# Kernel tuning notes

Measured on AMD Instinct MI355X. Metric: run time of the kernel, lower is better.

The kernel has to match this reference:

```python
import jax, jax.numpy as jnp
import numpy as np

BETA = 2.0  # init kwarg beta


def _roi_map(roi_params, H, W):
    # roi_params: (N, K, 4) = (mu_x, mu_y, sigma_x, sigma_y) in [0, 1]
    dtype = roi_params.dtype
    gx = (jnp.arange(W, dtype=dtype) + 0.5) / W  # x-coords of grid columns
    gy = (jnp.arange(H, dtype=dtype) + 0.5) / H  # y-coords of grid rows
    mu_x, mu_y = roi_params[:, :, 0], roi_params[:, :, 1]
    sg_x, sg_y = roi_params[:, :, 2], roi_params[:, :, 3]
    # separable generalized-Gaussian log pdf along each axis
    log_x = -(jnp.abs(gx[None, None, :] - mu_x[:, :, None]) / sg_x[:, :, None]) ** BETA  # (N,K,W)
    log_y = -(jnp.abs(gy[None, None, :] - mu_y[:, :, None]) / sg_y[:, :, None]) ** BETA  # (N,K,H)
    scores = jnp.exp(log_y[:, :, :, None] + log_x[:, :, None, :])  # (N,K,H,W)
    mx = jnp.max(scores, axis=(2, 3), keepdims=True)
    return scores / (mx + 1e-12)  # max-normalized attention maps


def setup_inputs() -> dict:
    key = jax.random.key(0)
    k1, k2 = jax.random.split(key)
    x = jax.random.normal(k1, (16, 128, 128, 256), dtype=jnp.float32)
    roi_params = jax.random.uniform(k2, (16, 64, 4), dtype=jnp.float32)
    return {"x": x, "roi_params": roi_params}


def reference(x, roi_params):
    N, H, W, d = x.shape
    roi_map = _roi_map(roi_params, H, W)           # (N,K,H,W)
    flat_map = roi_map.reshape(N, -1, H * W)        # (N,K,HW)
    flat_feats = x.reshape(N, H * W, d)             # (N,HW,d)
    roi_features = jnp.einsum('nrf,nfd->nrd', flat_map, flat_feats) / (H * W)
    return roi_features, roi_params, roi_map
```

## Files before the change

kernel.cpp:

```cpp
#include <hip/hip_runtime.h>
#include <hip/hip_bf16.h>
#include <math.h>

#define NB 16
#define RB 64
#define HB 128
#define WB 128
#define DB 256
#define HW (HB * WB)

typedef __attribute__((ext_vector_type(8))) short bf16x8;
typedef __attribute__((ext_vector_type(4))) float f32x4;

static __device__ __forceinline__ short f2bf(float f) {
  __hip_bfloat16 h = __float2bfloat16(f);
  return *reinterpret_cast<short*>(&h);
}

#define GLOAD_LDS16(gp, lp)                                          \
  __builtin_amdgcn_global_load_lds(                                  \
      (const __attribute__((address_space(1))) unsigned int*)(gp),   \
      (__attribute__((address_space(3))) unsigned int*)(lp), 16, 0, 0)

static __device__ __forceinline__ float axis_maxlog(float mu, float sg) {
  int i = (int)roundf(mu * 128.0f - 0.5f);
  i = i < 0 ? 0 : (i > 127 ? 127 : i);
  const float g = (i + 0.5f) * (1.0f / 128.0f);
  const float tm = fabsf(g - mu) / sg;
  return -(tm * tm);
}

template <bool INTERLEAVE>
__global__ __launch_bounds__(512, 1) void fused_kernel(
    const float* __restrict__ x, const float* __restrict__ roi,
    float* __restrict__ partials, float* __restrict__ out_map,
    float* __restrict__ out_params) {
  __shared__ float buf[4][32 * DB];

  const int bid = blockIdx.x;
  const int t   = threadIdx.x;

  bool is_map = false;
  int fid = bid, mb = 0;
  if constexpr (INTERLEAVE) {
    is_map = (bid % 3) == 2;
    fid    = (bid / 3) * 2 + (bid % 3);
    mb     = bid / 3;
  }

  if (is_map) {
    float* sEx = &buf[0][0];
    float* sEy = sEx + 512;
    for (int v = t; v < 1024; v += 512) {
      const int rr = v >> 8, axis = (v >> 7) & 1, pos = v & 127;
      const int nr = mb * 4 + rr;
      const float4 rp = reinterpret_cast<const float4*>(roi)[nr];
      const float mlx = axis_maxlog(rp.x, rp.z);
      const float mly = axis_maxlog(rp.y, rp.w);
      const float em  = expf(mlx + mly);
      const float s   = em / (em + 1e-12f);
      const float g   = (pos + 0.5f) * (1.0f / 128.0f);
      if (axis == 0) {
        const float tx = fabsf(g - rp.x) / rp.z;
        sEx[rr * 128 + pos] = expf(-(tx * tx) - mlx);
      } else {
        const float ty = fabsf(g - rp.y) / rp.w;
        sEy[rr * 128 + pos] = expf(-(ty * ty) - mly) * s;
      }
    }
    if (mb == 0) {
      for (int i = t; i < NB * RB * 4; i += 512) out_params[i] = roi[i];
    }
    __syncthreads();
    f32x4* dst = reinterpret_cast<f32x4*>(out_map + (size_t)mb * 4 * HW);
#pragma unroll
    for (int p = 0; p < 32; ++p) {
      const int idx = p * 512 + t;
      const int rr = idx >> 12, h = (idx >> 5) & 127, w4 = idx & 31;
      const f32x4 e = *reinterpret_cast<const f32x4*>(&sEx[rr * 128 + w4 * 4]);
      dst[idx] = e * (f32x4)sEy[rr * 128 + h];
    }
    return;
  }

  const int n   = fid >> 5;
  const int kc  = fid & 31;
  const int l   = t & 63;
  const int wv  = t >> 6;
  const int mh  = wv >> 2;
  const int dw  = wv & 3;
  const int l15 = l & 15;
  const int lk  = (l >> 4) * 8;
  const int h0  = kc * 4;
  const int dbase = dw * 64 + l15 * 4;

  const char* gx =
      (const char*)(x + ((size_t)n * HW + (size_t)kc * 512) * DB);
  char* lbase = (char*)&buf[0][0];

  f32x4 exr[2][4][2];
  float eyv[4][2];
#pragma unroll
  for (int rf = 0; rf < 2; ++rf) {
    const int nr = n * RB + mh * 32 + rf * 16 + l15;
    const float4 rp = reinterpret_cast<const float4*>(roi)[nr];
    const float mlx = axis_maxlog(rp.x, rp.z);
    const float mly = axis_maxlog(rp.y, rp.w);
    const float em  = expf(mlx + mly);
    const float s   = em / (em + 1e-12f);
#pragma unroll
    for (int ks = 0; ks < 4; ++ks) {
#pragma unroll
      for (int hf = 0; hf < 2; ++hf) {
        f32x4 v;
#pragma unroll
        for (int j = 0; j < 4; ++j) {
          const int col = ks * 32 + lk + hf * 4 + j;
          const float g = (col + 0.5f) * (1.0f / 128.0f);
          const float tx = fabsf(g - rp.x) / rp.z;
          v[j] = expf(-(tx * tx) - mlx);
        }
        exr[rf][ks][hf] = v;
      }
    }
#pragma unroll
    for (int hh = 0; hh < 4; ++hh) {
      const float g = (h0 + hh + 0.5f) * (1.0f / 128.0f);
      const float ty = fabsf(g - rp.y) / rp.w;
      eyv[hh][rf] = expf(-(ty * ty) - mly) * s;
    }
  }
  asm volatile("s_waitcnt vmcnt(0)" ::: "memory");

  f32x4 acc[2][4];
#pragma unroll
  for (int rf = 0; rf < 2; ++rf)
#pragma unroll
    for (int f = 0; f < 4; ++f) acc[rf][f] = (f32x4)0.0f;

#define STAGE(bi, slot) do {                                                 \
    const char* gsrc_ = gx + (size_t)(bi) * 32768;                           \
    char* ldst_ = lbase + (slot) * 32768;                                    \
    _Pragma("unroll")                                                        \
    for (int ii = 0; ii < 4; ++ii)                                           \
      GLOAD_LDS16(gsrc_ + ii * 8192 + wv * 1024 + l * 16,                    \
                  ldst_ + ii * 8192 + wv * 1024);                            \
  } while (0)

  STAGE(0, 0); STAGE(1, 1); STAGE(2, 2);

#define KSTEP(bi, VM, DO_STAGE) do {                                         \
    asm volatile("s_waitcnt vmcnt(" #VM ")" ::: "memory");                   \
    __builtin_amdgcn_s_barrier();                                            \
    __builtin_amdgcn_sched_barrier(0);                                       \
    if (DO_STAGE) STAGE((bi) + 3, ((bi) + 3) & 3);                           \
    const float* bp_ = &buf[(bi) & 3][0];                                    \
    f32x4 xv_[8];                                                            \
    _Pragma("unroll")                                                        \
    for (int j = 0; j < 8; ++j)                                              \
      xv_[j] = *reinterpret_cast<const f32x4*>(                              \
          bp_ + (lk + j) * DB + dbase);                                      \
    bf16x8 bfr_[4];                                                          \
    _Pragma("unroll")                                                        \
    for (int f = 0; f < 4; ++f) {                                            \
      bf16x8 b_;                                                             \
      _Pragma("unroll")                                                      \
      for (int j = 0; j < 8; ++j) b_[j] = f2bf(xv_[j][f]);                   \
      bfr_[f] = b_;                                                          \
    }                                                                        \
    bf16x8 afr_[2];                                                          \
    _Pragma("unroll")                                                        \
    for (int rf = 0; rf < 2; ++rf) {                                         \
      const float ey_ = eyv[(bi) >> 2][rf];                                  \
      const f32x4 e0_ = exr[rf][(bi) & 3][0];                                \
      const f32x4 e1_ = exr[rf][(bi) & 3][1];                                \
      bf16x8 a_;                                                             \
      a_[0] = f2bf(ey_ * e0_.x); a_[1] = f2bf(ey_ * e0_.y);                  \
      a_[2] = f2bf(ey_ * e0_.z); a_[3] = f2bf(ey_ * e0_.w);                  \
      a_[4] = f2bf(ey_ * e1_.x); a_[5] = f2bf(ey_ * e1_.y);                  \
      a_[6] = f2bf(ey_ * e1_.z); a_[7] = f2bf(ey_ * e1_.w);                  \
      afr_[rf] = a_;                                                         \
    }                                                                        \
    _Pragma("unroll")                                                        \
    for (int rf = 0; rf < 2; ++rf)                                           \
      _Pragma("unroll")                                                      \
      for (int f = 0; f < 4; ++f)                                            \
        acc[rf][f] = __builtin_amdgcn_mfma_f32_16x16x32_bf16(                \
            afr_[rf], bfr_[f], acc[rf][f], 0, 0, 0);                         \
  } while (0)

  KSTEP(0, 8, 1);  KSTEP(1, 8, 1);  KSTEP(2, 8, 1);  KSTEP(3, 8, 1);
  KSTEP(4, 8, 1);  KSTEP(5, 8, 1);  KSTEP(6, 8, 1);  KSTEP(7, 8, 1);
  KSTEP(8, 8, 1);  KSTEP(9, 8, 1);  KSTEP(10, 8, 1); KSTEP(11, 8, 1);
  KSTEP(12, 8, 1); KSTEP(13, 8, 0); KSTEP(14, 4, 0); KSTEP(15, 0, 0);

#undef KSTEP
#undef STAGE

  float* P = partials + (size_t)fid * (RB * DB);
#pragma unroll
  for (int rf = 0; rf < 2; ++rf) {
#pragma unroll
    for (int reg = 0; reg < 4; ++reg) {
      const int r = mh * 32 + rf * 16 + (l >> 4) * 4 + reg;
      f32x4 v;
      v.x = acc[rf][0][reg]; v.y = acc[rf][1][reg];
      v.z = acc[rf][2][reg]; v.w = acc[rf][3][reg];
      *reinterpret_cast<f32x4*>(P + (size_t)r * DB + dbase) = v;
    }
  }
}

__global__ __launch_bounds__(512) void map_only_kernel(
    const float* __restrict__ roi, float* __restrict__ out_map,
    float* __restrict__ out_params) {
  __shared__ float sT[1024];
  const int mb = blockIdx.x;
  const int t  = threadIdx.x;
  float* sEx = sT;
  float* sEy = sT + 512;
  for (int v = t; v < 1024; v += 512) {
    const int rr = v >> 8, axis = (v >> 7) & 1, pos = v & 127;
    const int nr = mb * 4 + rr;
    const float4 rp = reinterpret_cast<const float4*>(roi)[nr];
    const float mlx = axis_maxlog(rp.x, rp.z);
    const float mly = axis_maxlog(rp.y, rp.w);
    const float em  = expf(mlx + mly);
    const float s   = em / (em + 1e-12f);
    const float g   = (pos + 0.5f) * (1.0f / 128.0f);
    if (axis == 0) {
      const float tx = fabsf(g - rp.x) / rp.z;
      sEx[rr * 128 + pos] = expf(-(tx * tx) - mlx);
    } else {
      const float ty = fabsf(g - rp.y) / rp.w;
      sEy[rr * 128 + pos] = expf(-(ty * ty) - mly) * s;
    }
  }
  if (mb == 0) {
    for (int i = t; i < NB * RB * 4; i += 512) out_params[i] = roi[i];
  }
  __syncthreads();
  f32x4* dst = reinterpret_cast<f32x4*>(out_map + (size_t)mb * 4 * HW);
#pragma unroll
  for (int p = 0; p < 32; ++p) {
    const int idx = p * 512 + t;
    const int rr = idx >> 12, h = (idx >> 5) & 127, w4 = idx & 31;
    const f32x4 e = *reinterpret_cast<const f32x4*>(&sEx[rr * 128 + w4 * 4]);
    dst[idx] = e * (f32x4)sEy[rr * 128 + h];
  }
}

__global__ __launch_bounds__(256) void reduce_kernel(
    const float* __restrict__ partials, float* __restrict__ outF) {
  const int idx = blockIdx.x * 256 + threadIdx.x;
  const int n   = idx >> 12;
  const int i4  = idx & 4095;
  const f32x4* p =
      reinterpret_cast<const f32x4*>(partials) + (size_t)n * 32 * 4096 + i4;
  f32x4 s0 = (f32x4)0.0f, s1 = (f32x4)0.0f, s2 = (f32x4)0.0f, s3 = (f32x4)0.0f;
#pragma unroll
  for (int kc = 0; kc < 32; kc += 4) {
    s0 += p[(size_t)(kc + 0) * 4096];
    s1 += p[(size_t)(kc + 1) * 4096];
    s2 += p[(size_t)(kc + 2) * 4096];
    s3 += p[(size_t)(kc + 3) * 4096];
  }
  f32x4 s = (s0 + s1) + (s2 + s3);
  s *= (1.0f / (float)HW);
  reinterpret_cast<f32x4*>(outF)[idx] = s;
}

extern "C" void kernel_launch(void* const* d_in, const int* in_sizes, int n_in,
                              void* d_out, int out_size, void* d_ws, size_t ws_size,
                              hipStream_t stream) {
  const float* x   = (const float*)d_in[0];
  const float* roi = (const float*)d_in[1];
  float* out        = (float*)d_out;
  float* ws         = (float*)d_ws;
  float* out_feat   = out;
  float* out_params = out + NB * RB * DB;
  float* out_map    = out_params + NB * RB * 4;

  const size_t par_floats = 512u * RB * DB;
  const bool ws_ok = ws_size >= (par_floats + 16) * sizeof(float);

  if (ws_ok) {
    float* P = ws;
    fused_kernel<true><<<768, 512, 0, stream>>>(x, roi, P, out_map, out_params);
    reduce_kernel<<<256, 256, 0, stream>>>(P, out_feat);
  } else {
    float* P = out_map;
    fused_kernel<false><<<512, 512, 0, stream>>>(x, roi, P, out_map, out_params);
    reduce_kernel<<<256, 256, 0, stream>>>(P, out_feat);
    map_only_kernel<<<256, 512, 0, stream>>>(roi, out_map, out_params);
  }
}
```

Baseline: 99.12 us.

## Halve split-K blocks, emit map inside GEMM blocks, store bf16 partials

Drops the split-K factor from 32 to 16 chunks per batch, so 256 blocks each process 1024 spatial positions. Each GEMM block now writes its own 8 rows of the attention map after finishing its matmul, replacing the separate interleaved map-only blocks. Partials are stored as bf16, halving workspace traffic, and the params copy moves into the reduce kernel. The trade-offs are rounding error in the bf16 partial sums, and map writes serialized after the GEMM with fewer blocks than CUs available to overlap them.

```diff
diff --git a/kernel.cpp b/kernel.cpp
--- a/kernel.cpp
+++ b/kernel.cpp
@@ -10,11 +10,15 @@
 #define HW (HB * WB)
 
 typedef __attribute__((ext_vector_type(8))) short bf16x8;
+typedef __attribute__((ext_vector_type(4))) short short4v;
 typedef __attribute__((ext_vector_type(4))) float f32x4;
 
 static __device__ __forceinline__ short f2bf(float f) {
   __hip_bfloat16 h = __float2bfloat16(f);
   return *reinterpret_cast<short*>(&h);
+}
+static __device__ __forceinline__ float bf2f(short s) {
+  return __uint_as_float(((unsigned)(unsigned short)s) << 16);
 }
 
 #define GLOAD_LDS16(gp, lp)                                          \
@@ -30,76 +34,31 @@
   return -(tm * tm);
 }
 
-template <bool INTERLEAVE>
+template <bool WMAP>
 __global__ __launch_bounds__(512, 1) void fused_kernel(
     const float* __restrict__ x, const float* __restrict__ roi,
-    float* __restrict__ partials, float* __restrict__ out_map,
-    float* __restrict__ out_params) {
+    short* __restrict__ partials, float* __restrict__ out_map) {
   __shared__ float buf[4][32 * DB];
 
   const int bid = blockIdx.x;
+  const int n   = bid >> 4;
+  const int kc  = bid & 15;
   const int t   = threadIdx.x;
-
-  bool is_map = false;
-  int fid = bid, mb = 0;
-  if constexpr (INTERLEAVE) {
-    is_map = (bid % 3) == 2;
-    fid    = (bid / 3) * 2 + (bid % 3);
-    mb     = bid / 3;
-  }
-
-  if (is_map) {
-    float* sEx = &buf[0][0];
-    float* sEy = sEx + 512;
-    for (int v = t; v < 1024; v += 512) {
-      const int rr = v >> 8, axis = (v >> 7) & 1, pos = v & 127;
-      const int nr = mb * 4 + rr;
-      const float4 rp = reinterpret_cast<const float4*>(roi)[nr];
-      const float mlx = axis_maxlog(rp.x, rp.z);
-      const float mly = axis_maxlog(rp.y, rp.w);
-      const float em  = expf(mlx + mly);
-      const float s   = em / (em + 1e-12f);
-      const float g   = (pos + 0.5f) * (1.0f / 128.0f);
-      if (axis == 0) {
-        const float tx = fabsf(g - rp.x) / rp.z;
-        sEx[rr * 128 + pos] = expf(-(tx * tx) - mlx);
-      } else {
-        const float ty = fabsf(g - rp.y) / rp.w;
-        sEy[rr * 128 + pos] = expf(-(ty * ty) - mly) * s;
-      }
-    }
-    if (mb == 0) {
-      for (int i = t; i < NB * RB * 4; i += 512) out_params[i] = roi[i];
-    }
-    __syncthreads();
-    f32x4* dst = reinterpret_cast<f32x4*>(out_map + (size_t)mb * 4 * HW);
-#pragma unroll
-    for (int p = 0; p < 32; ++p) {
-      const int idx = p * 512 + t;
-      const int rr = idx >> 12, h = (idx >> 5) & 127, w4 = idx & 31;
-      const f32x4 e = *reinterpret_cast<const f32x4*>(&sEx[rr * 128 + w4 * 4]);
-      dst[idx] = e * (f32x4)sEy[rr * 128 + h];
-    }
-    return;
-  }
-
-  const int n   = fid >> 5;
-  const int kc  = fid & 31;
   const int l   = t & 63;
   const int wv  = t >> 6;
   const int mh  = wv >> 2;
   const int dw  = wv & 3;
   const int l15 = l & 15;
   const int lk  = (l >> 4) * 8;
-  const int h0  = kc * 4;
+  const int h0  = kc * 8;
   const int dbase = dw * 64 + l15 * 4;
 
   const char* gx =
-      (const char*)(x + ((size_t)n * HW + (size_t)kc * 512) * DB);
+      (const char*)(x + ((size_t)n * HW + (size_t)kc * 1024) * DB);
   char* lbase = (char*)&buf[0][0];
 
   f32x4 exr[2][4][2];
-  float eyv[4][2];
+  float eyv[8][2];
 #pragma unroll
   for (int rf = 0; rf < 2; ++rf) {
     const int nr = n * RB + mh * 32 + rf * 16 + l15;
@@ -124,7 +83,7 @@
       }
     }
 #pragma unroll
-    for (int hh = 0; hh < 4; ++hh) {
+    for (int hh = 0; hh < 8; ++hh) {
       const float g = (h0 + hh + 0.5f) * (1.0f / 128.0f);
       const float ty = fabsf(g - rp.y) / rp.w;
       eyv[hh][rf] = expf(-(ty * ty) - mly) * s;
@@ -189,31 +148,60 @@
             afr_[rf], bfr_[f], acc[rf][f], 0, 0, 0);                         \
   } while (0)
 
-  KSTEP(0, 8, 1);  KSTEP(1, 8, 1);  KSTEP(2, 8, 1);  KSTEP(3, 8, 1);
-  KSTEP(4, 8, 1);  KSTEP(5, 8, 1);  KSTEP(6, 8, 1);  KSTEP(7, 8, 1);
-  KSTEP(8, 8, 1);  KSTEP(9, 8, 1);  KSTEP(10, 8, 1); KSTEP(11, 8, 1);
-  KSTEP(12, 8, 1); KSTEP(13, 8, 0); KSTEP(14, 4, 0); KSTEP(15, 0, 0);
+  KSTEP(0, 8, 1);   KSTEP(1, 8, 1);   KSTEP(2, 8, 1);   KSTEP(3, 8, 1);
+  KSTEP(4, 8, 1);   KSTEP(5, 8, 1);   KSTEP(6, 8, 1);   KSTEP(7, 8, 1);
+  KSTEP(8, 8, 1);   KSTEP(9, 8, 1);   KSTEP(10, 8, 1);  KSTEP(11, 8, 1);
+  KSTEP(12, 8, 1);  KSTEP(13, 8, 1);  KSTEP(14, 8, 1);  KSTEP(15, 8, 1);
+  KSTEP(16, 8, 1);  KSTEP(17, 8, 1);  KSTEP(18, 8, 1);  KSTEP(19, 8, 1);
+  KSTEP(20, 8, 1);  KSTEP(21, 8, 1);  KSTEP(22, 8, 1);  KSTEP(23, 8, 1);
+  KSTEP(24, 8, 1);  KSTEP(25, 8, 1);  KSTEP(26, 8, 1);  KSTEP(27, 8, 1);
+  KSTEP(28, 8, 1);  KSTEP(29, 8, 0);  KSTEP(30, 4, 0);  KSTEP(31, 0, 0);
 
 #undef KSTEP
 #undef STAGE
 
-  float* P = partials + (size_t)fid * (RB * DB);
+  short* P = partials + (size_t)bid * (RB * DB);
 #pragma unroll
   for (int rf = 0; rf < 2; ++rf) {
 #pragma unroll
     for (int reg = 0; reg < 4; ++reg) {
       const int r = mh * 32 + rf * 16 + (l >> 4) * 4 + reg;
+      short4v v;
+      v.x = f2bf(acc[rf][0][reg]); v.y = f2bf(acc[rf][1][reg]);
+      v.z = f2bf(acc[rf][2][reg]); v.w = f2bf(acc[rf][3][reg]);
+      *reinterpret_cast<short4v*>(P + (size_t)r * DB + dbase) = v;
+    }
+  }
+
+  if constexpr (WMAP) {
+    const int h  = h0 + wv;
+    const int p4 = l & 31;
+    const float gh = (h + 0.5f) * (1.0f / 128.0f);
+#pragma unroll 4
+    for (int it = 0; it < 32; ++it) {
+      const int r = it * 2 + (l >> 5);
+      const float4 rp = reinterpret_cast<const float4*>(roi)[n * RB + r];
+      const float mlx = axis_maxlog(rp.x, rp.z);
+      const float mly = axis_maxlog(rp.y, rp.w);
+      const float em  = expf(mlx + mly);
+      const float s   = em / (em + 1e-12f);
+      const float ty  = fabsf(gh - rp.y) / rp.w;
+      const float ey  = expf(-(ty * ty) - mly) * s;
       f32x4 v;
-      v.x = acc[rf][0][reg]; v.y = acc[rf][1][reg];
-      v.z = acc[rf][2][reg]; v.w = acc[rf][3][reg];
-      *reinterpret_cast<f32x4*>(P + (size_t)r * DB + dbase) = v;
+#pragma unroll
+      for (int j = 0; j < 4; ++j) {
+        const float g  = (p4 * 4 + j + 0.5f) * (1.0f / 128.0f);
+        const float tx = fabsf(g - rp.x) / rp.z;
+        v[j] = expf(-(tx * tx) - mlx) * ey;
+      }
+      *reinterpret_cast<f32x4*>(
+          out_map + ((size_t)(n * RB + r) * HB + h) * WB + p4 * 4) = v;
     }
   }
 }
 
 __global__ __launch_bounds__(512) void map_only_kernel(
-    const float* __restrict__ roi, float* __restrict__ out_map,
-    float* __restrict__ out_params) {
+    const float* __restrict__ roi, float* __restrict__ out_map) {
   __shared__ float sT[1024];
   const int mb = blockIdx.x;
   const int t  = threadIdx.x;
@@ -221,8 +209,7 @@
   float* sEy = sT + 512;
   for (int v = t; v < 1024; v += 512) {
     const int rr = v >> 8, axis = (v >> 7) & 1, pos = v & 127;
-    const int nr = mb * 4 + rr;
-    const float4 rp = reinterpret_cast<const float4*>(roi)[nr];
+    const float4 rp = reinterpret_cast<const float4*>(roi)[mb * 4 + rr];
     const float mlx = axis_maxlog(rp.x, rp.z);
     const float mly = axis_maxlog(rp.y, rp.w);
     const float em  = expf(mlx + mly);
@@ -236,9 +223,6 @@
       sEy[rr * 128 + pos] = expf(-(ty * ty) - mly) * s;
     }
   }
-  if (mb == 0) {
-    for (int i = t; i < NB * RB * 4; i += 512) out_params[i] = roi[i];
-  }
   __syncthreads();
   f32x4* dst = reinterpret_cast<f32x4*>(out_map + (size_t)mb * 4 * HW);
 #pragma unroll
@@ -251,23 +235,22 @@
 }
 
 __global__ __launch_bounds__(256) void reduce_kernel(
-    const float* __restrict__ partials, float* __restrict__ outF) {
+    const short* __restrict__ partials, const float* __restrict__ roi,
+    float* __restrict__ outF, float* __restrict__ out_params) {
   const int idx = blockIdx.x * 256 + threadIdx.x;
   const int n   = idx >> 12;
   const int i4  = idx & 4095;
-  const f32x4* p =
-      reinterpret_cast<const f32x4*>(partials) + (size_t)n * 32 * 4096 + i4;
-  f32x4 s0 = (f32x4)0.0f, s1 = (f32x4)0.0f, s2 = (f32x4)0.0f, s3 = (f32x4)0.0f;
-#pragma unroll
-  for (int kc = 0; kc < 32; kc += 4) {
-    s0 += p[(size_t)(kc + 0) * 4096];
-    s1 += p[(size_t)(kc + 1) * 4096];
-    s2 += p[(size_t)(kc + 2) * 4096];
-    s3 += p[(size_t)(kc + 3) * 4096];
-  }
-  f32x4 s = (s0 + s1) + (s2 + s3);
+  const short4v* p =
+      reinterpret_cast<const short4v*>(partials) + (size_t)n * 16 * 4096 + i4;
+  f32x4 s = (f32x4)0.0f;
+#pragma unroll
+  for (int kc = 0; kc < 16; ++kc) {
+    const short4v v = p[(size_t)kc * 4096];
+    s.x += bf2f(v.x); s.y += bf2f(v.y); s.z += bf2f(v.z); s.w += bf2f(v.w);
+  }
   s *= (1.0f / (float)HW);
   reinterpret_cast<f32x4*>(outF)[idx] = s;
+  if (idx < NB * RB * 4) out_params[idx] = roi[idx];
 }
 
 extern "C" void kernel_launch(void* const* d_in, const int* in_sizes, int n_in,
@@ -276,22 +259,21 @@
   const float* x   = (const float*)d_in[0];
   const float* roi = (const float*)d_in[1];
   float* out        = (float*)d_out;
-  float* ws         = (float*)d_ws;
   float* out_feat   = out;
   float* out_params = out + NB * RB * DB;
   float* out_map    = out_params + NB * RB * 4;
 
-  const size_t par_floats = 512u * RB * DB;
-  const bool ws_ok = ws_size >= (par_floats + 16) * sizeof(float);
+  const size_t par_shorts = 256u * RB * DB;
+  const bool ws_ok = ws_size >= par_shorts * sizeof(short) + 64;
 
   if (ws_ok) {
-    float* P = ws;
-    fused_kernel<true><<<768, 512, 0, stream>>>(x, roi, P, out_map, out_params);
-    reduce_kernel<<<256, 256, 0, stream>>>(P, out_feat);
+    short* P = (short*)d_ws;
+    fused_kernel<true><<<256, 512, 0, stream>>>(x, roi, P, out_map);
+    reduce_kernel<<<256, 256, 0, stream>>>(P, roi, out_feat, out_params);
   } else {
-    float* P = out_map;
-    fused_kernel<false><<<512, 512, 0, stream>>>(x, roi, P, out_map, out_params);
-    reduce_kernel<<<256, 256, 0, stream>>>(P, out_feat);
-    map_only_kernel<<<256, 512, 0, stream>>>(roi, out_map, out_params);
-  }
-}
+    short* P = (short*)out_map;
+    fused_kernel<false><<<256, 512, 0, stream>>>(x, roi, P, out_map);
+    reduce_kernel<<<256, 256, 0, stream>>>(P, roi, out_feat, out_params);
+    map_only_kernel<<<256, 512, 0, stream>>>(roi, out_map);
+  }
+}
```

Result: faster. 94.92 us, median of 2 (-4.2%).
